# Kernel tuning notes

Measured on AMD Instinct MI355X. Metric: run time of the kernel, lower is better.

Reference implementation:

```python
import jax, jax.numpy as jnp
import numpy as np

B, N, F_IN, F_OUT = 4, 512, 64, 128


def setup_inputs() -> dict:
    key = jax.random.key(0)
    ks = jax.random.split(key, 12)
    def w(k, shape, fan_in):
        return (jax.random.normal(k, shape, jnp.float32) / np.sqrt(fan_in)).astype(jnp.float32)
    return {
        "nodes": jax.random.normal(ks[0], (B, N, F_IN), jnp.float32),
        "skeleton": jax.random.uniform(ks[1], (B, N, N, 1), jnp.float32),
        "edge_W": w(ks[2], (F_OUT, 2 * F_IN), 2 * F_IN),
        "edge_b": w(ks[3], (F_OUT,), 2 * F_IN),
        "node_W": w(ks[4], (F_OUT, F_OUT), F_OUT),
        "node_b": w(ks[5], (F_OUT,), F_OUT),
        "mlp_W0": w(ks[6], (F_OUT, F_IN), F_IN),
        "mlp_b0": w(ks[7], (F_OUT,), F_IN),
        "mlp_W1": w(ks[8], (F_OUT, F_OUT), F_OUT),
        "mlp_b1": w(ks[9], (F_OUT,), F_OUT),
        "mlp_W2": w(ks[10], (F_OUT, F_OUT), F_OUT),
        "mlp_b2": w(ks[11], (F_OUT,), F_OUT),
    }


def reference(nodes, skeleton, edge_W, edge_b, node_W, node_b,
              mlp_W0, mlp_b0, mlp_W1, mlp_b1, mlp_W2, mlp_b2):
    F = nodes.shape[-1]
    # nodes2edges: edge[b,i,j] = concat(nodes[b,j], nodes[b,i]).
    # Linear on concat splits into two small GEMMs + broadcast add (no [B,N,N,2F] tensor).
    pj = nodes @ edge_W[:, :F].T   # [B,N,F_out] contribution of node j (first half)
    pi = nodes @ edge_W[:, F:].T   # [B,N,F_out] contribution of node i (second half)
    edges = (pj[:, None, :, :] + pi[:, :, None, :] + edge_b) * skeleton  # [B,N,N,F_out]
    nodes_new = edges.sum(axis=1)                 # sum over i -> [B,N,F_out]
    nodes_new = nodes_new @ node_W.T + node_b
    # mlp: Linear-CELU-Linear-CELU-Linear
    h = jax.nn.celu(nodes @ mlp_W0.T + mlp_b0)
    h = jax.nn.celu(h @ mlp_W1.T + mlp_b1)
    h = h @ mlp_W2.T + mlp_b2
    return (h + nodes_new, edges)
```

## Files before the change

### kernel.cpp

```cpp
#include <hip/hip_runtime.h>
#include <cstddef>
#include <cstdint>

#define BB   4
#define NN   512
#define FIN  64
#define FOUT 128
#define PARTS 4
#define JT    4

typedef float f4 __attribute__((ext_vector_type(4)));

__device__ __forceinline__ float celu1(float x) {
  return x > 0.0f ? x : expm1f(x);
}

__global__ __launch_bounds__(FOUT) void k_proj(
    const float* __restrict__ nodes, const float* __restrict__ eW,
    const float* __restrict__ eb, float* __restrict__ pj,
    float* __restrict__ pip) {
  const int bn = blockIdx.x;
  const int f  = threadIdx.x;
  __shared__ __align__(16) float x[FIN];
  if (f < FIN) x[f] = nodes[bn * FIN + f];
  __syncthreads();
  const float* w = eW + f * (2 * FIN);
  float aj = 0.f, ai = 0.f;
#pragma unroll
  for (int k = 0; k < FIN; k += 4) {
    f4 xv = *(const f4*)(x + k);
    f4 wj = *(const f4*)(w + k);
    f4 wi = *(const f4*)(w + FIN + k);
    aj += wj.x * xv.x + wj.y * xv.y + wj.z * xv.z + wj.w * xv.w;
    ai += wi.x * xv.x + wi.y * xv.y + wi.z * xv.z + wi.w * xv.w;
  }
  pj[bn * FOUT + f]  = aj;
  pip[bn * FOUT + f] = ai + eb[f];
}

__global__ __launch_bounds__(128) void k_edges(
    const float* __restrict__ pj, const float* __restrict__ pip,
    const float* __restrict__ sk, float* __restrict__ edges,
    float* __restrict__ nn_part) {
  const int xb   = blockIdx.x;
  const int part = xb & (PARTS - 1);
  const int jt   = (xb >> 2) & (NN / JT - 1);
  const int b    = xb >> 9;

  const int g  = threadIdx.x >> 5;
  const int t  = threadIdx.x & 31;
  const int j  = jt * JT + g;
  const int fo = t * 4;
  const int i0 = part * (NN / PARTS);

  const f4 pjv = *(const f4*)(pj + (b * NN + j) * FOUT + fo);

  const float* pipp = pip + (b * NN + i0) * FOUT + fo;
  const float* skp  = sk + ((size_t)b * NN + i0) * NN + j;
  float*       ep   = edges + ((size_t)(b * NN + i0) * NN + j) * FOUT + fo;

  f4 acc = {0.f, 0.f, 0.f, 0.f};
  for (int i = 0; i < NN / PARTS; ++i) {
    f4 piv  = *(const f4*)pipp;
    float s = *skp;
    f4 v    = (pjv + piv) * s;
    __builtin_nontemporal_store(v, (f4*)ep);
    acc += v;
    pipp += FOUT;
    skp  += NN;
    ep   += (size_t)NN * FOUT;
  }
  *(f4*)(nn_part + ((size_t)(part * BB + b) * NN + j) * FOUT + fo) = acc;
}

__global__ __launch_bounds__(FOUT) void k_final(
    const float* __restrict__ nodes, const float* __restrict__ nn_part,
    const float* __restrict__ nW, const float* __restrict__ nb,
    const float* __restrict__ W0, const float* __restrict__ b0,
    const float* __restrict__ W1, const float* __restrict__ b1,
    const float* __restrict__ W2, const float* __restrict__ b2,
    float* __restrict__ out0) {
  const int bn = blockIdx.x;
  const int f  = threadIdx.x;
  __shared__ __align__(16) float x[FIN];
  __shared__ __align__(16) float r[FOUT];
  __shared__ __align__(16) float hA[FOUT];
  __shared__ __align__(16) float hB[FOUT];

  if (f < FIN) x[f] = nodes[bn * FIN + f];
  {
    float s = 0.f;
#pragma unroll
    for (int p = 0; p < PARTS; ++p)
      s += nn_part[((size_t)(p * BB * NN) + bn) * FOUT + f];
    r[f] = s;
  }
  __syncthreads();

  float s0 = b0[f];
  {
    const float* w = W0 + f * FIN;
#pragma unroll
    for (int k = 0; k < FIN; k += 4) {
      f4 wv = *(const f4*)(w + k);
      f4 xv = *(const f4*)(x + k);
      s0 += wv.x * xv.x + wv.y * xv.y + wv.z * xv.z + wv.w * xv.w;
    }
  }
  hA[f] = celu1(s0);
  __syncthreads();

  float s1 = b1[f];
  {
    const float* w = W1 + f * FOUT;
#pragma unroll
    for (int k = 0; k < FOUT; k += 4) {
      f4 wv = *(const f4*)(w + k);
      f4 hv = *(const f4*)(hA + k);
      s1 += wv.x * hv.x + wv.y * hv.y + wv.z * hv.z + wv.w * hv.w;
    }
  }
  float nv = nb[f];
  {
    const float* w = nW + f * FOUT;
#pragma unroll
    for (int k = 0; k < FOUT; k += 4) {
      f4 wv = *(const f4*)(w + k);
      f4 rv = *(const f4*)(r + k);
      nv += wv.x * rv.x + wv.y * rv.y + wv.z * rv.z + wv.w * rv.w;
    }
  }
  hB[f] = celu1(s1);
  __syncthreads();

  float s2 = b2[f];
  {
    const float* w = W2 + f * FOUT;
#pragma unroll
    for (int k = 0; k < FOUT; k += 4) {
      f4 wv = *(const f4*)(w + k);
      f4 hv = *(const f4*)(hB + k);
      s2 += wv.x * hv.x + wv.y * hv.y + wv.z * hv.z + wv.w * hv.w;
    }
  }
  out0[bn * FOUT + f] = s2 + nv;
}

extern "C" void kernel_launch(void* const* d_in, const int* in_sizes, int n_in,
                              void* d_out, int out_size, void* d_ws,
                              size_t ws_size, hipStream_t stream) {
  const float* nodes    = (const float*)d_in[0];
  const float* skeleton = (const float*)d_in[1];
  const float* edge_W   = (const float*)d_in[2];
  const float* edge_b   = (const float*)d_in[3];
  const float* node_W   = (const float*)d_in[4];
  const float* node_b   = (const float*)d_in[5];
  const float* mlp_W0   = (const float*)d_in[6];
  const float* mlp_b0   = (const float*)d_in[7];
  const float* mlp_W1   = (const float*)d_in[8];
  const float* mlp_b1   = (const float*)d_in[9];
  const float* mlp_W2   = (const float*)d_in[10];
  const float* mlp_b2   = (const float*)d_in[11];

  float* out0  = (float*)d_out;
  float* edges = out0 + (size_t)BB * NN * FOUT;

  float* ws      = (float*)d_ws;
  float* pj      = ws;
  float* pip     = ws + (size_t)BB * NN * FOUT;
  float* nn_part = ws + (size_t)2 * BB * NN * FOUT;

  k_proj<<<BB * NN, FOUT, 0, stream>>>(nodes, edge_W, edge_b, pj, pip);
  k_edges<<<BB * (NN / JT) * PARTS, 128, 0, stream>>>(pj, pip, skeleton, edges,
                                                      nn_part);
  k_final<<<BB * NN, FOUT, 0, stream>>>(nodes, nn_part, node_W, node_b, mlp_W0,
                                        mlp_b0, mlp_W1, mlp_b1, mlp_W2, mlp_b2,
                                        out0);
}
```

Measured before the change: 653.6 us.

## Stage pip rows and skeleton in LDS with double-buffered prefetch in edge kernel

The edge kernel now loads its block's skeleton slice into shared memory once, with coalesced loads, instead of each thread doing strided scalar reads. The pip rows are staged through a double-buffered shared-memory tile of 16 rows, and the next chunk is prefetched into registers while the current one is processed. This removes scattered global loads and overlaps load latency with the streaming edge stores, at the cost of extra LDS use, barriers and register pressure. The kernel is dominated by writing the large edges output, so the gain may be limited.

```diff
diff --git a/kernel.cpp b/kernel.cpp
--- a/kernel.cpp
+++ b/kernel.cpp
@@ -8,6 +8,8 @@
 #define FOUT 128
 #define PARTS 4
 #define JT    4
+#define CCH  16
+#define NCH  ((NN / PARTS) / CCH)
 
 typedef float f4 __attribute__((ext_vector_type(4)));
 
@@ -47,29 +49,78 @@
   const int jt   = (xb >> 2) & (NN / JT - 1);
   const int b    = xb >> 9;
 
-  const int g  = threadIdx.x >> 5;
-  const int t  = threadIdx.x & 31;
-  const int j  = jt * JT + g;
-  const int fo = t * 4;
-  const int i0 = part * (NN / PARTS);
+  const int tid = threadIdx.x;
+  const int g   = tid >> 5;
+  const int t   = tid & 31;
+  const int j   = jt * JT + g;
+  const int fo  = t * 4;
+  const int i0  = part * (NN / PARTS);
+
+  __shared__ __align__(16) float lpip[2][CCH][FOUT];
+  __shared__ __align__(16) float lsk[NN / PARTS][JT];
+
+  {
+    const float* skb = sk + ((size_t)b * NN + i0) * NN + jt * JT;
+#pragma unroll
+    for (int r = 0; r < (NN / PARTS) * JT / 128; ++r) {
+      const int idx = tid + 128 * r;
+      const int ii  = idx >> 2;
+      const int gg  = idx & 3;
+      lsk[ii][gg] = skb[(size_t)ii * NN + gg];
+    }
+  }
 
   const f4 pjv = *(const f4*)(pj + (b * NN + j) * FOUT + fo);
 
-  const float* pipp = pip + (b * NN + i0) * FOUT + fo;
-  const float* skp  = sk + ((size_t)b * NN + i0) * NN + j;
-  float*       ep   = edges + ((size_t)(b * NN + i0) * NN + j) * FOUT + fo;
+  const float* pipb = pip + ((size_t)b * NN + i0) * FOUT;
+  float* ep = edges + ((size_t)(b * NN + i0) * NN + j) * FOUT + fo;
+
+  {
+    f4 r0 = *(const f4*)(pipb + 4 * tid);
+    f4 r1 = *(const f4*)(pipb + 4 * tid + 512);
+    f4 r2 = *(const f4*)(pipb + 4 * tid + 1024);
+    f4 r3 = *(const f4*)(pipb + 4 * tid + 1536);
+    float* ld = &lpip[0][0][0];
+    *(f4*)(ld + 4 * tid)        = r0;
+    *(f4*)(ld + 4 * tid + 512)  = r1;
+    *(f4*)(ld + 4 * tid + 1024) = r2;
+    *(f4*)(ld + 4 * tid + 1536) = r3;
+  }
+  __syncthreads();
 
   f4 acc = {0.f, 0.f, 0.f, 0.f};
-  for (int i = 0; i < NN / PARTS; ++i) {
-    f4 piv  = *(const f4*)pipp;
-    float s = *skp;
-    f4 v    = (pjv + piv) * s;
-    __builtin_nontemporal_store(v, (f4*)ep);
-    acc += v;
-    pipp += FOUT;
-    skp  += NN;
-    ep   += (size_t)NN * FOUT;
-  }
+  for (int ch = 0; ch < NCH; ++ch) {
+    const int cb = ch & 1;
+
+    f4 n0, n1, n2, n3;
+    if (ch + 1 < NCH) {
+      const float* pc = pipb + (size_t)(ch + 1) * CCH * FOUT;
+      n0 = *(const f4*)(pc + 4 * tid);
+      n1 = *(const f4*)(pc + 4 * tid + 512);
+      n2 = *(const f4*)(pc + 4 * tid + 1024);
+      n3 = *(const f4*)(pc + 4 * tid + 1536);
+    }
+
+#pragma unroll
+    for (int c = 0; c < CCH; ++c) {
+      f4 piv  = *(const f4*)(&lpip[cb][c][fo]);
+      float s = lsk[ch * CCH + c][g];
+      f4 v    = (pjv + piv) * s;
+      acc += v;
+      __builtin_nontemporal_store(v, (f4*)ep);
+      ep += (size_t)NN * FOUT;
+    }
+
+    if (ch + 1 < NCH) {
+      float* ld = &lpip[cb ^ 1][0][0];
+      *(f4*)(ld + 4 * tid)        = n0;
+      *(f4*)(ld + 4 * tid + 512)  = n1;
+      *(f4*)(ld + 4 * tid + 1024) = n2;
+      *(f4*)(ld + 4 * tid + 1536) = n3;
+    }
+    __syncthreads();
+  }
+
   *(f4*)(nn_part + ((size_t)(part * BB + b) * NN + j) * FOUT + fo) = acc;
 }
 
```

Measured after the change: 631.8 us. 1.03x faster.

## Restructure edge kernel for coalesced row writes and move node reduction to final kernel

Applied to the files above, without the earlier changes.

The edge kernel now tiles 16 i-rows by 256 j-columns per 512-thread block. It stages the skeleton and pip tiles in shared memory and keeps 16 pj vectors in registers, so each thread writes contiguous edge rows instead of striding across i. The reduction over i is taken out of the edge kernel. The final kernel instead recomputes it directly from pj, pip and skeleton with a column-strided skeleton read. Regular stores replace nontemporal stores. This removes the partial-sum buffer, but the final kernel now does about 512 extra FMA steps per element and uncoalesced skeleton loads.

```diff
diff --git a/kernel.cpp b/kernel.cpp
--- a/kernel.cpp
+++ b/kernel.cpp
@@ -6,8 +6,11 @@
 #define NN   512
 #define FIN  64
 #define FOUT 128
-#define PARTS 4
-#define JT    4
+
+#define IPARTS 32
+#define IBLK   (NN / IPARTS)
+#define JH     (NN / 2)
+#define TE     512
 
 typedef float f4 __attribute__((ext_vector_type(4)));
 
@@ -38,64 +41,93 @@
   pip[bn * FOUT + f] = ai + eb[f];
 }
 
-__global__ __launch_bounds__(128) void k_edges(
+__global__ __launch_bounds__(TE) void k_edges(
     const float* __restrict__ pj, const float* __restrict__ pip,
-    const float* __restrict__ sk, float* __restrict__ edges,
-    float* __restrict__ nn_part) {
-  const int xb   = blockIdx.x;
-  const int part = xb & (PARTS - 1);
-  const int jt   = (xb >> 2) & (NN / JT - 1);
-  const int b    = xb >> 9;
-
-  const int g  = threadIdx.x >> 5;
-  const int t  = threadIdx.x & 31;
-  const int j  = jt * JT + g;
-  const int fo = t * 4;
-  const int i0 = part * (NN / PARTS);
-
-  const f4 pjv = *(const f4*)(pj + (b * NN + j) * FOUT + fo);
-
-  const float* pipp = pip + (b * NN + i0) * FOUT + fo;
-  const float* skp  = sk + ((size_t)b * NN + i0) * NN + j;
-  float*       ep   = edges + ((size_t)(b * NN + i0) * NN + j) * FOUT + fo;
-
-  f4 acc = {0.f, 0.f, 0.f, 0.f};
-  for (int i = 0; i < NN / PARTS; ++i) {
-    f4 piv  = *(const f4*)pipp;
-    float s = *skp;
-    f4 v    = (pjv + piv) * s;
-    __builtin_nontemporal_store(v, (f4*)ep);
-    acc += v;
-    pipp += FOUT;
-    skp  += NN;
-    ep   += (size_t)NN * FOUT;
-  }
-  *(f4*)(nn_part + ((size_t)(part * BB + b) * NN + j) * FOUT + fo) = acc;
+    const float* __restrict__ sk, float* __restrict__ edges) {
+  const int xb  = blockIdx.x;
+  const int ip  = xb & 31;
+  const int jhf = (xb >> 5) & 1;
+  const int b   = xb >> 6;
+  const int tid = threadIdx.x;
+  const int i0  = ip * IBLK;
+  const int j0  = jhf * JH;
+
+  __shared__ __align__(16) float lsk[IBLK][JH];
+  __shared__ __align__(16) float lpip[IBLK][FOUT];
+
+  const int jl = tid >> 5;
+  const int f0 = (tid & 31) * 4;
+
+  f4 pjr[16];
+  {
+    const float* src = pj + ((size_t)b * NN + j0) * FOUT;
+#pragma unroll
+    for (int s = 0; s < 16; ++s)
+      pjr[s] = *(const f4*)(src + (s * 16 + jl) * FOUT + f0);
+  }
+  {
+    const float* src = pip + ((size_t)b * NN + i0) * FOUT;
+    *(f4*)(&lpip[0][0] + tid * 4) = *(const f4*)(src + tid * 4);
+  }
+  {
+#pragma unroll
+    for (int r = 0; r < 8; ++r) {
+      const int idx = r * TE + tid;
+      const int ii  = idx >> 8;
+      const int jj  = idx & 255;
+      lsk[ii][jj] = sk[((size_t)b * NN + i0 + ii) * NN + j0 + jj];
+    }
+  }
+  __syncthreads();
+
+  float* ep = edges + (((size_t)(b * NN + i0)) * NN + j0) * FOUT;
+#pragma unroll 1
+  for (int ii = 0; ii < IBLK; ++ii) {
+    const f4 piv = *(const f4*)(&lpip[ii][f0]);
+#pragma unroll
+    for (int s = 0; s < 16; ++s) {
+      const float sv = lsk[ii][s * 16 + jl];
+      f4 v = (pjr[s] + piv) * sv;
+      *(f4*)(ep + (size_t)s * (16 * FOUT) + tid * 4) = v;
+    }
+    ep += (size_t)NN * FOUT;
+  }
 }
 
 __global__ __launch_bounds__(FOUT) void k_final(
-    const float* __restrict__ nodes, const float* __restrict__ nn_part,
+    const float* __restrict__ nodes, const float* __restrict__ pj,
+    const float* __restrict__ pip, const float* __restrict__ sk,
     const float* __restrict__ nW, const float* __restrict__ nb,
     const float* __restrict__ W0, const float* __restrict__ b0,
     const float* __restrict__ W1, const float* __restrict__ b1,
     const float* __restrict__ W2, const float* __restrict__ b2,
     float* __restrict__ out0) {
   const int bn = blockIdx.x;
+  const int b  = bn >> 9;
+  const int j  = bn & (NN - 1);
   const int f  = threadIdx.x;
+
   __shared__ __align__(16) float x[FIN];
-  __shared__ __align__(16) float r[FOUT];
+  __shared__ __align__(16) float lsk[NN];
+  __shared__ __align__(16) float rL[FOUT];
   __shared__ __align__(16) float hA[FOUT];
   __shared__ __align__(16) float hB[FOUT];
 
   if (f < FIN) x[f] = nodes[bn * FIN + f];
-  {
-    float s = 0.f;
-#pragma unroll
-    for (int p = 0; p < PARTS; ++p)
-      s += nn_part[((size_t)(p * BB * NN) + bn) * FOUT + f];
-    r[f] = s;
-  }
-  __syncthreads();
+#pragma unroll
+  for (int p = 0; p < 4; ++p)
+    lsk[f + 128 * p] = sk[((size_t)b * NN + f + 128 * p) * NN + j];
+  __syncthreads();
+
+  float r = 0.f;
+  {
+    const float pjv = pj[(b * NN + j) * FOUT + f];
+    const float* pb = pip + (size_t)b * NN * FOUT + f;
+#pragma unroll 8
+    for (int i = 0; i < NN; ++i)
+      r += (pjv + pb[(size_t)i * FOUT]) * lsk[i];
+  }
+  rL[f] = r;
 
   float s0 = b0[f];
   {
@@ -126,7 +158,7 @@
 #pragma unroll
     for (int k = 0; k < FOUT; k += 4) {
       f4 wv = *(const f4*)(w + k);
-      f4 rv = *(const f4*)(r + k);
+      f4 rv = *(const f4*)(rL + k);
       nv += wv.x * rv.x + wv.y * rv.y + wv.z * rv.z + wv.w * rv.w;
     }
   }
@@ -165,15 +197,13 @@
   float* out0  = (float*)d_out;
   float* edges = out0 + (size_t)BB * NN * FOUT;
 
-  float* ws      = (float*)d_ws;
-  float* pj      = ws;
-  float* pip     = ws + (size_t)BB * NN * FOUT;
-  float* nn_part = ws + (size_t)2 * BB * NN * FOUT;
+  float* ws  = (float*)d_ws;
+  float* pj  = ws;
+  float* pip = ws + (size_t)BB * NN * FOUT;
 
   k_proj<<<BB * NN, FOUT, 0, stream>>>(nodes, edge_W, edge_b, pj, pip);
-  k_edges<<<BB * (NN / JT) * PARTS, 128, 0, stream>>>(pj, pip, skeleton, edges,
-                                                      nn_part);
-  k_final<<<BB * NN, FOUT, 0, stream>>>(nodes, nn_part, node_W, node_b, mlp_W0,
-                                        mlp_b0, mlp_W1, mlp_b1, mlp_W2, mlp_b2,
-                                        out0);
-}
+  k_edges<<<BB * 2 * IPARTS, TE, 0, stream>>>(pj, pip, skeleton, edges);
+  k_final<<<BB * NN, FOUT, 0, stream>>>(nodes, pj, pip, skeleton, node_W,
+                                        node_b, mlp_W0, mlp_b0, mlp_W1, mlp_b1,
+                                        mlp_W2, mlp_b2, out0);
+}
```

New measurement: 730.9 us. 11.8% more time.
